# Kernel tuning notes

Measured on AMD Instinct MI355X. Metric: run time of the kernel, lower is better.

## Reference

```python
import jax, jax.numpy as jnp
import numpy as np

B, T, D, N = 8, 2000, 64, 2000
ALPHA = 1.0


def setup_inputs() -> dict:
    key = jax.random.key(0)
    k1, k2, k3, k4 = jax.random.split(key, 4)
    x = jax.random.normal(k1, (B, T, D), dtype=jnp.float32)
    Win = jax.random.normal(k2, (D, N), dtype=jnp.float32) * 0.1
    # dense random reservoir matrix scaled to spectral-radius-like magnitude
    Wres = jax.random.normal(k3, (N, N), dtype=jnp.float32) * (0.6 / np.sqrt(N))
    Wout = jax.random.normal(k4, (N, D), dtype=jnp.float32) * 0.05
    return {"x": x, "Win": Win, "Wres": Wres, "Wout": Wout}


def reference(x, Win, Wres, Wout):
    # x: [B, T, D]; leaky-integrated ESN reservoir recurrence over time.
    n = Wres.shape[0]
    init_state = jnp.zeros((x.shape[0], n), dtype=x.dtype)  # [B, N]

    def step(state, x_t):
        cand = jnp.tanh(state @ Wres + x_t @ Win)          # [B, N]
        new_state = state + ALPHA * (cand - state)          # leaky update
        return new_state, new_state

    xs = jnp.swapaxes(x, 0, 1)                              # [T, B, D]
    _, states = jax.lax.scan(step, init_state, xs)          # [T, B, N]
    h = jnp.swapaxes(states, 0, 1)                          # [B, T, N]
    # square every even-indexed reservoir feature (Lu/Pathak augmentation)
    even_mask = (jnp.arange(n) % 2 == 0)
    h = jnp.where(even_mask, h * h, h)
    return h @ Wout                                         # [B, T, D]
```

## Files before the change

kernel.cpp:

```cpp
#include <hip/hip_runtime.h>

#define BB 8
#define TT 2000
#define DD 64
#define NN 2000
#define NWG 125
#define COLS 16
#define THREADS 512
#define SROW 2048
#define XST 68

#define LDS_BYTES (65536 + 4352 + 4096)

typedef __bf16 bf16x8 __attribute__((ext_vector_type(8)));
typedef float f32x4 __attribute__((ext_vector_type(4)));

__device__ __forceinline__ float fast_tanh(float v) {
    float e = __expf(2.0f * v);
    return 1.0f - 2.0f / (e + 1.0f);
}

__device__ __forceinline__ uint4 ld_uc4(const void* p) {
    uint4 v;
    asm volatile("global_load_dwordx4 %0, %1, off sc0 sc1" : "=v"(v) : "v"(p) : "memory");
    return v;
}
__device__ __forceinline__ void st_uc_u16(void* p, unsigned v) {
    asm volatile("global_store_short %0, %1, off sc0 sc1" :: "v"(p), "v"(v) : "memory");
}
__device__ __forceinline__ void st_uc_u32(void* p, unsigned v) {
    asm volatile("global_store_dword %0, %1, off sc0 sc1" :: "v"(p), "v"(v) : "memory");
}

__device__ __forceinline__ void poll_ge_pipelined(const unsigned* p, unsigned tgt) {
    unsigned a, b;
    asm volatile(
        "global_load_dword %0, %2, off sc0 sc1\n\t"
        "global_load_dword %1, %2, off sc0 sc1\n\t"
        "Lp_%=:\n\t"
        "s_waitcnt vmcnt(1)\n\t"
        "v_cmp_le_u32 vcc, %3, %0\n\t"
        "s_cbranch_vccnz Ld_%=\n\t"
        "global_load_dword %0, %2, off sc0 sc1\n\t"
        "s_waitcnt vmcnt(1)\n\t"
        "v_cmp_le_u32 vcc, %3, %1\n\t"
        "s_cbranch_vccnz Ld_%=\n\t"
        "global_load_dword %1, %2, off sc0 sc1\n\t"
        "s_branch Lp_%=\n\t"
        "Ld_%=:\n\t"
        "s_waitcnt vmcnt(0)\n\t"
        : "=&v"(a), "=&v"(b)
        : "v"(p), "v"(tgt)
        : "vcc", "memory");
}

__device__ __forceinline__ void sweep_all_ge(const unsigned* p0, const unsigned* p1,
                                             unsigned tgt) {
    unsigned a, b, c, d;
    unsigned long long sm;
    asm volatile(
        "global_load_dword %0, %5, off sc0 sc1\n\t"
        "global_load_dword %1, %6, off sc0 sc1\n\t"
        "global_load_dword %2, %5, off sc0 sc1\n\t"
        "global_load_dword %3, %6, off sc0 sc1\n\t"
        "Ls_%=:\n\t"
        "s_waitcnt vmcnt(2)\n\t"
        "v_cmp_le_u32 vcc, %7, %0\n\t"
        "s_mov_b64 %4, vcc\n\t"
        "v_cmp_le_u32 vcc, %7, %1\n\t"
        "s_and_b64 %4, %4, vcc\n\t"
        "s_xor_b64 %4, %4, exec\n\t"
        "s_cbranch_scc0 Ld_%=\n\t"
        "global_load_dword %0, %5, off sc0 sc1\n\t"
        "global_load_dword %1, %6, off sc0 sc1\n\t"
        "s_waitcnt vmcnt(2)\n\t"
        "v_cmp_le_u32 vcc, %7, %2\n\t"
        "s_mov_b64 %4, vcc\n\t"
        "v_cmp_le_u32 vcc, %7, %3\n\t"
        "s_and_b64 %4, %4, vcc\n\t"
        "s_xor_b64 %4, %4, exec\n\t"
        "s_cbranch_scc0 Ld_%=\n\t"
        "global_load_dword %2, %5, off sc0 sc1\n\t"
        "global_load_dword %3, %6, off sc0 sc1\n\t"
        "s_branch Ls_%=\n\t"
        "Ld_%=:\n\t"
        "s_waitcnt vmcnt(0)\n\t"
        : "=&v"(a), "=&v"(b), "=&v"(c), "=&v"(d), "=&s"(sm)
        : "v"(p0), "v"(p1), "v"(tgt)
        : "vcc", "memory");
}


__global__ void __launch_bounds__(THREADS, 1)
esn_recur(const float* __restrict__ x, const float* __restrict__ Win,
          const float* __restrict__ Wres, char* __restrict__ sgB,
          float* __restrict__ H, unsigned* __restrict__ flags,
          unsigned* __restrict__ gen)
{
    extern __shared__ char smraw[];
    __bf16* wS   = (__bf16*)smraw;
    float*  winS = (float*)(wS + 16 * SROW);
    float*  red  = winS + 16 * XST;

    const int tid  = threadIdx.x;
    const int wg   = blockIdx.x;
    const int col0 = wg * COLS;
    const int wave = tid >> 6;
    const int lane = tid & 63;

    for (int i = tid; i < LDS_BYTES / 4; i += THREADS) ((unsigned*)smraw)[i] = 0u;
    __syncthreads();

    {
        const int c = tid & 15, h = c & 7;
        for (int k = tid >> 4; k < NN; k += 32)
            wS[c * SROW + ((((k >> 3) ^ h) << 3) | (k & 7))] =
                (__bf16)Wres[(size_t)k * NN + col0 + c];
    }
    for (int i = tid; i < COLS * DD; i += THREADS) {
        int c = i >> 6, d = i & 63;
        winS[c * XST + d] = Win[(size_t)d * NN + col0 + c];
    }
    __syncthreads();

    const int quad = lane >> 4;
    const int bcol = lane & 15;
    const int hb   = bcol & 7;
    const int fb = lane >> 4, fc = lane & 15;
    const int cg = col0 + fc;
    const int pReg = cg >> 5, pSub = (cg >> 3) & 3, pJ = (cg & 7) * 2;
    const size_t pOff0 = (((size_t)(pReg * 32 + pSub * 8 + fb    )) << 4) + pJ;
    const size_t pOff1 = (((size_t)(pReg * 32 + pSub * 8 + fb + 4)) << 4) + pJ;
    const size_t aLane = (size_t)((quad * 8 + (lane & 7)) << 4);
    const unsigned* f1 = flags + lane;
    const unsigned* f2 = flags + ((lane < 61) ? (64 + lane) : 0);

    unsigned bw[8][4];
    {
        const __bf16* bBase = wS + bcol * SROW;
        const int blk0 = wave * 32 + quad;
        #pragma unroll
        for (int m = 0; m < 8; ++m) {
            uint4 v = *(const uint4*)(bBase + (((blk0 + m * 4) ^ hb) << 3));
            bw[m][0] = v.x; bw[m][1] = v.y; bw[m][2] = v.z; bw[m][3] = v.w;
            asm volatile("" : "+v"(bw[m][0]), "+v"(bw[m][1]),
                              "+v"(bw[m][2]), "+v"(bw[m][3]));
        }
    }

    for (int t = 0; t < TT; ++t) {
        float xa0 = 0.f, xa1 = 0.f;
        if (wave == 1) {
            const float4* xr0 = (const float4*)(x + ((size_t)fb * TT + t) * DD);
            const float4* xr1 = (const float4*)(x + ((size_t)(fb + 4) * TT + t) * DD);
            const float4* wv  = (const float4*)(winS + fc * XST);
            #pragma unroll
            for (int d4 = 0; d4 < 16; ++d4) {
                float4 w = wv[d4];
                float4 u0 = xr0[d4], u1 = xr1[d4];
                xa0 = fmaf(u0.x, w.x, xa0); xa0 = fmaf(u0.y, w.y, xa0);
                xa0 = fmaf(u0.z, w.z, xa0); xa0 = fmaf(u0.w, w.w, xa0);
                xa1 = fmaf(u1.x, w.x, xa1); xa1 = fmaf(u1.y, w.y, xa1);
                xa1 = fmaf(u1.z, w.z, xa1); xa1 = fmaf(u1.w, w.w, xa1);
            }
        }

        f32x4 acc = {0.f, 0.f, 0.f, 0.f};
        if (t > 0) {
            const unsigned tgt = (unsigned)t;
            if (wave == 0) {
                if (wg == 0) {
                    sweep_all_ge(f1, f2, tgt);
                    if (lane == 0) st_uc_u32(gen, tgt);
                } else if (lane == 0) {
                    poll_ge_pipelined(gen, tgt);
                }
            }
            __builtin_amdgcn_s_barrier();

            const char* aB = sgB + (size_t)(t & 1) * 32768 + wave * 4096 + aLane;
            uint4 a0 = ld_uc4(aB);
            uint4 a1 = ld_uc4(aB + 512);
            uint4 a2 = ld_uc4(aB + 1024);
            uint4 a3 = ld_uc4(aB + 1536);
            uint4 a4 = ld_uc4(aB + 2048);
            uint4 a5 = ld_uc4(aB + 2560);
            uint4 a6 = ld_uc4(aB + 3072);
            uint4 a7 = ld_uc4(aB + 3584);
            asm volatile("s_waitcnt vmcnt(0)" ::: "memory");
            __builtin_amdgcn_sched_barrier(0);

            #define MSTEP(mm, areg) { \
                uint4 bu = make_uint4(bw[mm][0], bw[mm][1], bw[mm][2], bw[mm][3]); \
                acc = __builtin_amdgcn_mfma_f32_16x16x32_bf16( \
                    __builtin_bit_cast(bf16x8, areg), \
                    __builtin_bit_cast(bf16x8, bu), acc, 0, 0, 0); }
            MSTEP(0, a0) MSTEP(1, a1) MSTEP(2, a2) MSTEP(3, a3)
            MSTEP(4, a4) MSTEP(5, a5) MSTEP(6, a6) MSTEP(7, a7)
            #undef MSTEP
        }
        if (lane < 32) {
            const int r0 = (lane >> 4) * 4;
            #pragma unroll
            for (int i = 0; i < 4; ++i)
                red[(wave * 8 + r0 + i) * 16 + bcol] = acc[i];
        }
        __syncthreads();

        if (wave == 1) {
            float a0s = xa0, a1s = xa1;
            #pragma unroll
            for (int w = 0; w < 8; ++w) {
                a0s += red[(w * 8 + fb    ) * 16 + fc];
                a1s += red[(w * 8 + fb + 4) * 16 + fc];
            }
            float s0 = fast_tanh(a0s);
            float s1 = fast_tanh(a1s);
            if (t < TT - 1) {
                __bf16 b0 = (__bf16)s0, b1 = (__bf16)s1;
                unsigned short u0, u1;
                __builtin_memcpy(&u0, &b0, 2);
                __builtin_memcpy(&u1, &b1, 2);
                char* dstG = sgB + (size_t)((t + 1) & 1) * 32768;
                st_uc_u16(dstG + pOff0, (unsigned)u0);
                st_uc_u16(dstG + pOff1, (unsigned)u1);
                asm volatile("s_waitcnt vmcnt(0)" ::: "memory");
                if (lane == 0) st_uc_u32(flags + wg, (unsigned)(t + 1));
            }
            float h0 = (fc & 1) ? s0 : s0 * s0;
            float h1 = (fc & 1) ? s1 : s1 * s1;
            H[((size_t)t * BB + fb    ) * NN + col0 + fc] = h0;
            H[((size_t)t * BB + fb + 4) * NN + col0 + fc] = h1;
        }
    }
}

__global__ void __launch_bounds__(256, 1)
esn_out(const float* __restrict__ H, const float* __restrict__ Wout,
        float* __restrict__ out)
{
    __shared__ float Hs[64 * 84];
    __shared__ float Ws[80 * 64];
    const int tid = threadIdx.x;
    const int r0  = blockIdx.x * 64;
    const int tr  = tid >> 4;
    const int tc  = tid & 15;
    float acc[4][4] = {{0.f}};

    for (int k0 = 0; k0 < NN; k0 += 80) {
        __syncthreads();
        #pragma unroll
        for (int j = 0; j < 5; ++j) {
            int idx = j * 256 + tid;
            int r = idx / 20, q = idx % 20;
            *(float4*)&Hs[r * 84 + q * 4] =
                *(const float4*)&H[(size_t)(r0 + r) * NN + k0 + q * 4];
        }
        #pragma unroll
        for (int j = 0; j < 5; ++j) {
            int idx = j * 256 + tid;
            int kk = idx >> 4, c4 = idx & 15;
            *(float4*)&Ws[kk * 64 + c4 * 4] =
                *(const float4*)&Wout[(size_t)(k0 + kk) * DD + c4 * 4];
        }
        __syncthreads();
        for (int kk = 0; kk < 80; ++kk) {
            float4 wv = *(const float4*)&Ws[kk * 64 + tc * 4];
            #pragma unroll
            for (int i = 0; i < 4; ++i) {
                float hv = Hs[(tr + 16 * i) * 84 + kk];
                acc[i][0] = fmaf(hv, wv.x, acc[i][0]);
                acc[i][1] = fmaf(hv, wv.y, acc[i][1]);
                acc[i][2] = fmaf(hv, wv.z, acc[i][2]);
                acc[i][3] = fmaf(hv, wv.w, acc[i][3]);
            }
        }
    }
    #pragma unroll
    for (int i = 0; i < 4; ++i) {
        int rg = r0 + tr + 16 * i;
        int t = rg >> 3, b = rg & 7;
        *(float4*)&out[((size_t)b * TT + t) * DD + tc * 4] =
            make_float4(acc[i][0], acc[i][1], acc[i][2], acc[i][3]);
    }
}

extern "C" void kernel_launch(void* const* d_in, const int* in_sizes, int n_in,
                              void* d_out, int out_size, void* d_ws, size_t ws_size,
                              hipStream_t stream)
{
    const float* x    = (const float*)d_in[0];
    const float* Win  = (const float*)d_in[1];
    const float* Wres = (const float*)d_in[2];
    const float* Wout = (const float*)d_in[3];
    float* out = (float*)d_out;

    char* ws = (char*)d_ws;
    unsigned* flags = (unsigned*)ws;
    unsigned* gen   = (unsigned*)(ws + 2048);
    char* sG  = ws + 4096;
    float* H  = (float*)(ws + 4096 + 65536);

    (void)hipMemsetAsync(d_ws, 0, 4096 + 65536, stream);

    (void)hipFuncSetAttribute((const void*)esn_recur,
                              hipFuncAttributeMaxDynamicSharedMemorySize, LDS_BYTES);
    esn_recur<<<NWG, THREADS, LDS_BYTES, stream>>>(x, Win, Wres, sG, H, flags, gen);
    esn_out<<<250, 256, 0, stream>>>(H, Wout, out);
}
```

Measured before the change: 6.155 ms.

## Replace centralized flag-gather barrier with replicated per-group flag arrays

The old scheme had one master workgroup sweep all 125 flags and then publish a generation counter that the other workgroups polled, so each step paid two serial global-memory round trips. Now each workgroup writes its step flag into 8 replicated flag rows, and every workgroup sweeps one replica directly with 32 lanes loading 4 flags each, which removes the master relay hop. The cost is 8 stores per step per workgroup and polling traffic from all 125 workgroups spread over 8 replicas. The padding slots past index 125 are pre-set to 0xFF so the sweep comparison passes on them.

```diff
diff --git a/kernel.cpp b/kernel.cpp
--- a/kernel.cpp
+++ b/kernel.cpp
@@ -32,61 +32,55 @@
     asm volatile("global_store_dword %0, %1, off sc0 sc1" :: "v"(p), "v"(v) : "memory");
 }
 
-__device__ __forceinline__ void poll_ge_pipelined(const unsigned* p, unsigned tgt) {
-    unsigned a, b;
+__device__ __forceinline__ void sweep4_pipelined(const unsigned* p, unsigned tgt) {
+    unsigned a0, a1, a2, a3, b0, b1, b2, b3;
+    unsigned long long m;
     asm volatile(
-        "global_load_dword %0, %2, off sc0 sc1\n\t"
-        "global_load_dword %1, %2, off sc0 sc1\n\t"
-        "Lp_%=:\n\t"
-        "s_waitcnt vmcnt(1)\n\t"
-        "v_cmp_le_u32 vcc, %3, %0\n\t"
-        "s_cbranch_vccnz Ld_%=\n\t"
-        "global_load_dword %0, %2, off sc0 sc1\n\t"
-        "s_waitcnt vmcnt(1)\n\t"
-        "v_cmp_le_u32 vcc, %3, %1\n\t"
-        "s_cbranch_vccnz Ld_%=\n\t"
-        "global_load_dword %1, %2, off sc0 sc1\n\t"
-        "s_branch Lp_%=\n\t"
-        "Ld_%=:\n\t"
-        "s_waitcnt vmcnt(0)\n\t"
-        : "=&v"(a), "=&v"(b)
-        : "v"(p), "v"(tgt)
-        : "vcc", "memory");
-}
-
-__device__ __forceinline__ void sweep_all_ge(const unsigned* p0, const unsigned* p1,
-                                             unsigned tgt) {
-    unsigned a, b, c, d;
-    unsigned long long sm;
-    asm volatile(
-        "global_load_dword %0, %5, off sc0 sc1\n\t"
-        "global_load_dword %1, %6, off sc0 sc1\n\t"
-        "global_load_dword %2, %5, off sc0 sc1\n\t"
-        "global_load_dword %3, %6, off sc0 sc1\n\t"
+        "global_load_dword %0, %9, off sc0 sc1\n\t"
+        "global_load_dword %1, %9, off offset:4 sc0 sc1\n\t"
+        "global_load_dword %2, %9, off offset:8 sc0 sc1\n\t"
+        "global_load_dword %3, %9, off offset:12 sc0 sc1\n\t"
+        "global_load_dword %4, %9, off sc0 sc1\n\t"
+        "global_load_dword %5, %9, off offset:4 sc0 sc1\n\t"
+        "global_load_dword %6, %9, off offset:8 sc0 sc1\n\t"
+        "global_load_dword %7, %9, off offset:12 sc0 sc1\n\t"
         "Ls_%=:\n\t"
-        "s_waitcnt vmcnt(2)\n\t"
-        "v_cmp_le_u32 vcc, %7, %0\n\t"
-        "s_mov_b64 %4, vcc\n\t"
-        "v_cmp_le_u32 vcc, %7, %1\n\t"
-        "s_and_b64 %4, %4, vcc\n\t"
-        "s_xor_b64 %4, %4, exec\n\t"
+        "s_waitcnt vmcnt(4)\n\t"
+        "v_cmp_le_u32 vcc, %10, %0\n\t"
+        "s_mov_b64 %8, vcc\n\t"
+        "v_cmp_le_u32 vcc, %10, %1\n\t"
+        "s_and_b64 %8, %8, vcc\n\t"
+        "v_cmp_le_u32 vcc, %10, %2\n\t"
+        "s_and_b64 %8, %8, vcc\n\t"
+        "v_cmp_le_u32 vcc, %10, %3\n\t"
+        "s_and_b64 %8, %8, vcc\n\t"
+        "s_xor_b64 %8, %8, exec\n\t"
         "s_cbranch_scc0 Ld_%=\n\t"
-        "global_load_dword %0, %5, off sc0 sc1\n\t"
-        "global_load_dword %1, %6, off sc0 sc1\n\t"
-        "s_waitcnt vmcnt(2)\n\t"
-        "v_cmp_le_u32 vcc, %7, %2\n\t"
-        "s_mov_b64 %4, vcc\n\t"
-        "v_cmp_le_u32 vcc, %7, %3\n\t"
-        "s_and_b64 %4, %4, vcc\n\t"
-        "s_xor_b64 %4, %4, exec\n\t"
+        "global_load_dword %0, %9, off sc0 sc1\n\t"
+        "global_load_dword %1, %9, off offset:4 sc0 sc1\n\t"
+        "global_load_dword %2, %9, off offset:8 sc0 sc1\n\t"
+        "global_load_dword %3, %9, off offset:12 sc0 sc1\n\t"
+        "s_waitcnt vmcnt(4)\n\t"
+        "v_cmp_le_u32 vcc, %10, %4\n\t"
+        "s_mov_b64 %8, vcc\n\t"
+        "v_cmp_le_u32 vcc, %10, %5\n\t"
+        "s_and_b64 %8, %8, vcc\n\t"
+        "v_cmp_le_u32 vcc, %10, %6\n\t"
+        "s_and_b64 %8, %8, vcc\n\t"
+        "v_cmp_le_u32 vcc, %10, %7\n\t"
+        "s_and_b64 %8, %8, vcc\n\t"
+        "s_xor_b64 %8, %8, exec\n\t"
         "s_cbranch_scc0 Ld_%=\n\t"
-        "global_load_dword %2, %5, off sc0 sc1\n\t"
-        "global_load_dword %3, %6, off sc0 sc1\n\t"
+        "global_load_dword %4, %9, off sc0 sc1\n\t"
+        "global_load_dword %5, %9, off offset:4 sc0 sc1\n\t"
+        "global_load_dword %6, %9, off offset:8 sc0 sc1\n\t"
+        "global_load_dword %7, %9, off offset:12 sc0 sc1\n\t"
         "s_branch Ls_%=\n\t"
         "Ld_%=:\n\t"
         "s_waitcnt vmcnt(0)\n\t"
-        : "=&v"(a), "=&v"(b), "=&v"(c), "=&v"(d), "=&s"(sm)
-        : "v"(p0), "v"(p1), "v"(tgt)
+        : "=&v"(a0), "=&v"(a1), "=&v"(a2), "=&v"(a3),
+          "=&v"(b0), "=&v"(b1), "=&v"(b2), "=&v"(b3), "=&s"(m)
+        : "v"(p), "v"(tgt)
         : "vcc", "memory");
 }
 
@@ -94,8 +88,7 @@
 __global__ void __launch_bounds__(THREADS, 1)
 esn_recur(const float* __restrict__ x, const float* __restrict__ Win,
           const float* __restrict__ Wres, char* __restrict__ sgB,
-          float* __restrict__ H, unsigned* __restrict__ flags,
-          unsigned* __restrict__ gen)
+          float* __restrict__ H, unsigned* __restrict__ frep)
 {
     extern __shared__ char smraw[];
     __bf16* wS   = (__bf16*)smraw;
@@ -132,8 +125,8 @@
     const size_t pOff0 = (((size_t)(pReg * 32 + pSub * 8 + fb    )) << 4) + pJ;
     const size_t pOff1 = (((size_t)(pReg * 32 + pSub * 8 + fb + 4)) << 4) + pJ;
     const size_t aLane = (size_t)((quad * 8 + (lane & 7)) << 4);
-    const unsigned* f1 = flags + lane;
-    const unsigned* f2 = flags + ((lane < 61) ? (64 + lane) : 0);
+    const unsigned* swp = frep + (wg & 7) * 128 + lane * 4;
+    unsigned* fdst = frep + lane * 128 + wg;
 
     unsigned bw[8][4];
     {
@@ -167,14 +160,8 @@
 
         f32x4 acc = {0.f, 0.f, 0.f, 0.f};
         if (t > 0) {
-            const unsigned tgt = (unsigned)t;
-            if (wave == 0) {
-                if (wg == 0) {
-                    sweep_all_ge(f1, f2, tgt);
-                    if (lane == 0) st_uc_u32(gen, tgt);
-                } else if (lane == 0) {
-                    poll_ge_pipelined(gen, tgt);
-                }
+            if (wave == 0 && lane < 32) {
+                sweep4_pipelined(swp, (unsigned)t);
             }
             __builtin_amdgcn_s_barrier();
 
@@ -225,7 +212,7 @@
                 st_uc_u16(dstG + pOff0, (unsigned)u0);
                 st_uc_u16(dstG + pOff1, (unsigned)u1);
                 asm volatile("s_waitcnt vmcnt(0)" ::: "memory");
-                if (lane == 0) st_uc_u32(flags + wg, (unsigned)(t + 1));
+                if (lane < 8) st_uc_u32(fdst, (unsigned)(t + 1));
             }
             float h0 = (fc & 1) ? s0 : s0 * s0;
             float h1 = (fc & 1) ? s1 : s1 * s1;
@@ -296,15 +283,16 @@
     float* out = (float*)d_out;
 
     char* ws = (char*)d_ws;
-    unsigned* flags = (unsigned*)ws;
-    unsigned* gen   = (unsigned*)(ws + 2048);
+    unsigned* frep = (unsigned*)ws;
     char* sG  = ws + 4096;
     float* H  = (float*)(ws + 4096 + 65536);
 
     (void)hipMemsetAsync(d_ws, 0, 4096 + 65536, stream);
+    for (int r = 0; r < 8; ++r)
+        (void)hipMemsetAsync(ws + r * 512 + 500, 0xFF, 12, stream);
 
     (void)hipFuncSetAttribute((const void*)esn_recur,
                               hipFuncAttributeMaxDynamicSharedMemorySize, LDS_BYTES);
-    esn_recur<<<NWG, THREADS, LDS_BYTES, stream>>>(x, Win, Wres, sG, H, flags, gen);
+    esn_recur<<<NWG, THREADS, LDS_BYTES, stream>>>(x, Win, Wres, sG, H, frep);
     esn_out<<<250, 256, 0, stream>>>(H, Wout, out);
 }
```

New measurement: 7.416 ms. +20.5%, slower.
